# Kernel tuning notes

Measured on AMD Instinct MI355X. Metric: run time of the kernel, lower is better.

Reference implementation:

```python
import jax, jax.numpy as jnp
import numpy as np

B, S, H = 8, 1024, 1024
NH, HD = 16, 64
LN_EPS = 1e-12


def setup_inputs() -> dict:
    key = jax.random.key(0)
    ks = jax.random.split(key, 8)
    sd = 0.02
    return {
        "hidden_states": jax.random.normal(ks[0], (B, S, H), jnp.float32),
        "attention_mask": jnp.zeros((B, 1, 1, S), jnp.float32),
        "Wq": jax.random.normal(ks[1], (H, H), jnp.float32) * sd,
        "bq": jnp.zeros((H,), jnp.float32),
        "Wk": jax.random.normal(ks[2], (H, H), jnp.float32) * sd,
        "bk": jnp.zeros((H,), jnp.float32),
        "Wv": jax.random.normal(ks[3], (H, H), jnp.float32) * sd,
        "bv": jnp.zeros((H,), jnp.float32),
        "Wo": jax.random.normal(ks[4], (H, H), jnp.float32) * sd,
        "bo": jnp.zeros((H,), jnp.float32),
        "ln_gamma": jnp.ones((H,), jnp.float32),
        "ln_beta": jnp.zeros((H,), jnp.float32),
    }


def _heads(x):
    # [B,S,H] -> [B,NH,S,HD]
    return x.reshape(B, S, NH, HD).transpose(0, 2, 1, 3)


def reference(hidden_states, attention_mask, Wq, bq, Wk, bk, Wv, bv, Wo, bo, ln_gamma, ln_beta):
    # QKV projections (torch Linear: x @ W.T + b)
    q = _heads(hidden_states @ Wq.T + bq)
    k = _heads(hidden_states @ Wk.T + bk)
    v = _heads(hidden_states @ Wv.T + bv)
    # scaled dot-product attention with additive mask
    scores = jnp.einsum("bhqd,bhkd->bhqk", q, k) / np.sqrt(HD).astype(np.float32)
    scores = scores + attention_mask  # broadcast [B,1,1,S]
    probs = jax.nn.softmax(scores, axis=-1)
    ctx = jnp.einsum("bhqk,bhkd->bhqd", probs, v)
    ctx = ctx.transpose(0, 2, 1, 3).reshape(B, S, H)
    # output projection + residual + LayerNorm
    out = ctx @ Wo.T + bo
    x = out + hidden_states
    mu = jnp.mean(x, axis=-1, keepdims=True)
    var = jnp.var(x, axis=-1, keepdims=True)
    return (x - mu) * jax.lax.rsqrt(var + LN_EPS) * ln_gamma + ln_beta
```

## Files before the change

kernel.cpp:

```cpp
#include <hip/hip_runtime.h>
#include <stdint.h>

typedef __attribute__((ext_vector_type(8))) __bf16 bf16x8;
typedef __attribute__((ext_vector_type(8))) unsigned short ushortx8;
typedef __attribute__((ext_vector_type(4))) unsigned short ushortx4;
typedef __attribute__((ext_vector_type(4))) short short4v;
typedef __attribute__((ext_vector_type(4))) float floatx4;

#define LOG2E 1.4426950408889634f
#define QSCALE 0.18033688011112043f

#define ASYNC16(g, l) __builtin_amdgcn_global_load_lds( \
    (__attribute__((address_space(1))) void*)(g),       \
    (__attribute__((address_space(3))) void*)(l), 16, 0, 0)

__device__ __forceinline__ unsigned short f2bf(float f) {
    unsigned int u = __float_as_uint(f);
    u += 0x7fffu + ((u >> 16) & 1u);
    return (unsigned short)(u >> 16);
}
__device__ __forceinline__ float bf2f(unsigned short u) {
    return __uint_as_float((unsigned)u << 16);
}

__device__ __forceinline__ floatx4 mfma32(bf16x8 a, bf16x8 b, floatx4 c) {
    return __builtin_amdgcn_mfma_f32_16x16x32_bf16(a, b, c, 0, 0, 0);
}
__device__ __forceinline__ floatx4 mfma16(short4v a, short4v b, floatx4 c) {
    return __builtin_amdgcn_mfma_f32_16x16x16bf16_1k(a, b, c, 0, 0, 0);
}

__global__ __launch_bounds__(256) void cvt_all(
    const float* __restrict__ hidden,
    const float* __restrict__ Wq, const float* __restrict__ Wk,
    const float* __restrict__ Wv, const float* __restrict__ Wo,
    unsigned short* __restrict__ hid_bf,
    unsigned short* __restrict__ oqkv, unsigned short* __restrict__ oo)
{
    const float* src;
    unsigned short* dst;
    int i;
    if (blockIdx.x < 4096) {
        src = hidden; dst = hid_bf;
        i = blockIdx.x * 256 + threadIdx.x;
    } else {
        int blk = (blockIdx.x - 4096) >> 9;
        src = (blk == 0) ? Wq : (blk == 1) ? Wk : (blk == 2) ? Wv : Wo;
        dst = (blk == 3) ? oo : oqkv + (size_t)blk * 1048576;
        i = ((blockIdx.x - 4096) & 511) * 256 + threadIdx.x;
    }
    const float4* p = (const float4*)src + (size_t)i * 2;
    float4 a = p[0], b = p[1];
    ushortx8 o;
    o[0] = f2bf(a.x); o[1] = f2bf(a.y); o[2] = f2bf(a.z); o[3] = f2bf(a.w);
    o[4] = f2bf(b.x); o[5] = f2bf(b.y); o[6] = f2bf(b.z); o[7] = f2bf(b.w);
    *((ushortx8*)dst + i) = o;
}

template<bool SWAP>
__device__ __forceinline__ void kloop_bk64(
    const unsigned short* __restrict__ Ag,
    const unsigned short* __restrict__ Wg,
    unsigned short* As, unsigned short* Bs,
    int wm, int wn, int l16, int quad, int t,
    floatx4 acc[4][4])
{
#pragma unroll 1
    for (int k0 = 0; k0 < 1024; k0 += 64) {
        __syncthreads();
#pragma unroll
        for (int i = 0; i < 4; i++) {
            ASYNC16(Ag + (size_t)i * 32 * 1024 + k0, As + i * 2048 + t * 8);
            ASYNC16(Wg + (size_t)i * 32 * 1024 + k0, Bs + i * 2048 + t * 8);
        }
        __syncthreads();
#pragma unroll
        for (int s = 0; s < 2; s++) {
            int pb = ((s * 4 + quad) ^ (l16 & 7)) * 8;
            bf16x8 af[4], bfr[4];
#pragma unroll
            for (int mt = 0; mt < 4; mt++)
                af[mt] = *(const bf16x8*)(As + (wm + mt * 16 + l16) * 64 + pb);
#pragma unroll
            for (int nt = 0; nt < 4; nt++)
                bfr[nt] = *(const bf16x8*)(Bs + (wn + nt * 16 + l16) * 64 + pb);
            if (SWAP) {
#pragma unroll
                for (int ft = 0; ft < 4; ft++)
#pragma unroll
                    for (int st = 0; st < 4; st++)
                        acc[ft][st] = mfma32(bfr[ft], af[st], acc[ft][st]);
            } else {
#pragma unroll
                for (int mt = 0; mt < 4; mt++)
#pragma unroll
                    for (int nt = 0; nt < 4; nt++)
                        acc[mt][nt] = mfma32(af[mt], bfr[nt], acc[mt][nt]);
            }
        }
    }
}

__global__ __launch_bounds__(512, 2) void gemm_qkv(
    const unsigned short* __restrict__ A,
    const unsigned short* __restrict__ W,
    const float* __restrict__ bq, const float* __restrict__ bk, const float* __restrict__ bv,
    unsigned short* __restrict__ Qo, unsigned short* __restrict__ Ko,
    unsigned short* __restrict__ Vo)
{
    __shared__ unsigned short As[2][16384];
    __shared__ unsigned short Bs[2][12288];
    const int t = threadIdx.x;
    const int lane = t & 63, quad = lane >> 4, l16 = lane & 15;
    const int wid = t >> 6;
    const int wm = (wid >> 2) * 128;
    const int wn = (wid & 3) * 48;
    const int rr = t >> 3;
    const int cc = ((t & 7) ^ (rr & 7)) * 8;
    const int t8 = t * 8;

    const unsigned short* Ab = A + ((size_t)blockIdx.x * 256 + rr) * 1024 + cc;
    const unsigned short* Wb = W + ((size_t)blockIdx.y * 192 + rr) * 1024 + cc;

#define SA(bf_, u_, kt_) ASYNC16(Ab + (size_t)(u_) * 65536 + (kt_) * 64, &As[bf_][(u_) * 4096 + t8])
#define SB(bf_, u_, kt_) ASYNC16(Wb + (size_t)(u_) * 65536 + (kt_) * 64, &Bs[bf_][(u_) * 4096 + t8])

    SA(0, 0, 0); SA(0, 1, 0); SA(0, 2, 0); SA(0, 3, 0);
    SB(0, 0, 0); SB(0, 1, 0); SB(0, 2, 0);
    SB(1, 0, 1); SB(1, 1, 1); SB(1, 2, 1); SA(1, 0, 1); SA(1, 2, 1);
    asm volatile("s_waitcnt vmcnt(5)" ::: "memory");
    __builtin_amdgcn_s_barrier();

    floatx4 acc[3][8] = {};

#pragma unroll 1
    for (int kt = 0; kt < 16; ++kt) {
        const int cur = kt & 1, nb = cur ^ 1;
        const unsigned short* Ac = As[cur];
        const unsigned short* Bc = Bs[cur];
        bf16x8 bfr[3][2];
        bf16x8 af[4][2];

#pragma unroll
        for (int j = 0; j < 4; ++j)
#pragma unroll
            for (int s = 0; s < 2; ++s)
                af[j][s] = *(const bf16x8*)(Ac + (wm + j * 16 + l16) * 64 +
                                            ((s * 4 + quad) ^ (l16 & 7)) * 8);
#pragma unroll
        for (int ft = 0; ft < 3; ++ft)
#pragma unroll
            for (int s = 0; s < 2; ++s)
                bfr[ft][s] = *(const bf16x8*)(Bc + (wn + ft * 16 + l16) * 64 +
                                              ((s * 4 + quad) ^ (l16 & 7)) * 8);
        if (kt < 15) { SA(nb, 1, kt + 1); SA(nb, 3, kt + 1); }
        __builtin_amdgcn_s_barrier();
        asm volatile("s_waitcnt lgkmcnt(0)" ::: "memory");
        __builtin_amdgcn_sched_barrier(0);
        __builtin_amdgcn_s_setprio(1);
#pragma unroll
        for (int ft = 0; ft < 3; ++ft)
#pragma unroll
            for (int j = 0; j < 4; ++j) {
                acc[ft][j] = mfma32(bfr[ft][0], af[j][0], acc[ft][j]);
                acc[ft][j] = mfma32(bfr[ft][1], af[j][1], acc[ft][j]);
            }
        __builtin_amdgcn_s_setprio(0);
        __builtin_amdgcn_s_barrier();

#pragma unroll
        for (int j = 0; j < 4; ++j)
#pragma unroll
            for (int s = 0; s < 2; ++s)
                af[j][s] = *(const bf16x8*)(Ac + (wm + 64 + j * 16 + l16) * 64 +
                                            ((s * 4 + quad) ^ (l16 & 7)) * 8);
        if (kt < 14) {
            SB(cur, 0, kt + 2); SB(cur, 1, kt + 2); SB(cur, 2, kt + 2);
            SA(cur, 0, kt + 2); SA(cur, 2, kt + 2);
        }
        __builtin_amdgcn_s_barrier();
        asm volatile("s_waitcnt lgkmcnt(0)" ::: "memory");
        __builtin_amdgcn_sched_barrier(0);
        __builtin_amdgcn_s_setprio(1);
#pragma unroll
        for (int ft = 0; ft < 3; ++ft)
#pragma unroll
            for (int j = 0; j < 4; ++j) {
                acc[ft][4 + j] = mfma32(bfr[ft][0], af[j][0], acc[ft][4 + j]);
                acc[ft][4 + j] = mfma32(bfr[ft][1], af[j][1], acc[ft][4 + j]);
            }
        __builtin_amdgcn_s_setprio(0);
        if (kt < 14)       { asm volatile("s_waitcnt vmcnt(5)" ::: "memory"); }
        else if (kt == 14) { asm volatile("s_waitcnt vmcnt(0)" ::: "memory"); }
        if (kt < 15) __builtin_amdgcn_s_barrier();
    }
#undef SA
#undef SB

#pragma unroll
    for (int ft = 0; ft < 3; ++ft) {
        const int featg = blockIdx.y * 192 + wn + ft * 16 + quad * 4;
        const int mat = featg >> 10;
        const int fin = featg & 1023;
        if (mat < 2) {
            const float* bp = (mat == 0) ? bq : bk;
            unsigned short* op = (mat == 0) ? Qo : Ko;
            const float sc = (mat == 0) ? QSCALE : 1.0f;
            const float4 b4 = *(const float4*)(bp + fin);
            const int h = fin >> 6, d = fin & 63;
#pragma unroll
            for (int st = 0; st < 8; ++st) {
                const int sg = blockIdx.x * 256 + wm + st * 16 + l16;
                const int b = sg >> 10, s = sg & 1023;
                ushortx4 o4;
                o4[0] = f2bf((acc[ft][st][0] + b4.x) * sc);
                o4[1] = f2bf((acc[ft][st][1] + b4.y) * sc);
                o4[2] = f2bf((acc[ft][st][2] + b4.z) * sc);
                o4[3] = f2bf((acc[ft][st][3] + b4.w) * sc);
                *(ushortx4*)(op + (((size_t)(b * 16 + h) * 1024 + s) * 64 + d)) = o4;
            }
        } else {
            const float4 b4 = *(const float4*)(bv + fin);
#pragma unroll
            for (int r = 0; r < 4; ++r) {
                const int fr = fin + r;
                const int h = fr >> 6, d = fr & 63;
                const float bias = (r == 0) ? b4.x : (r == 1) ? b4.y : (r == 2) ? b4.z : b4.w;
#pragma unroll
                for (int st = 0; st < 8; ++st) {
                    const int sg = blockIdx.x * 256 + wm + st * 16 + l16;
                    const int b = sg >> 10, s = sg & 1023;
                    const int sp = (s & ~63) + ((st >> 1) & 1) * 32 + (l16 >> 2) * 8 +
                                   (st & 1) * 4 + (l16 & 3);
                    Vo[((size_t)(b * 16 + h) * 64 + d) * 1024 + sp] = f2bf(acc[ft][st][r] + bias);
                }
            }
        }
    }
}

__global__ __launch_bounds__(256) void attn(
    const unsigned short* __restrict__ Q,
    const unsigned short* __restrict__ Kg,
    const unsigned short* __restrict__ Vt,
    const float* __restrict__ mask,
    unsigned short* __restrict__ ctx)
{
    __shared__ unsigned short Ks[64 * 64];
    __shared__ unsigned short Vs[64 * 64];
    __shared__ float Msall[1024];

    const int t = threadIdx.x;
    const int wave = t >> 6, lane = t & 63, quad = lane >> 4, l16 = lane & 15;
    const int s7 = l16 & 7;
    const int head = blockIdx.x;
    const int b = head >> 4, h = head & 15;
    const int q0 = blockIdx.y * 128;
    const unsigned short* Qh = Q + (size_t)head * 65536;
    const unsigned short* Kh = Kg + (size_t)head * 65536;
    const unsigned short* Vh = Vt + (size_t)head * 65536;

    const int srow = t >> 3;
    const int scol = ((t & 7) ^ (srow & 7)) * 8;

    {
        float4 m4 = *(const float4*)(mask + b * 1024 + t * 4);
        m4.x *= LOG2E; m4.y *= LOG2E; m4.z *= LOG2E; m4.w *= LOG2E;
        *(float4*)(Msall + t * 4) = m4;
    }

    bf16x8 qf[2][2];
#pragma unroll
    for (int qg = 0; qg < 2; qg++) {
        const unsigned short* qp = Qh + (size_t)(q0 + wave * 32 + qg * 16 + l16) * 64 + quad * 8;
        qf[qg][0] = *(const bf16x8*)(qp);
        qf[qg][1] = *(const bf16x8*)(qp + 32);
    }

    const short4v ones = {(short)0x3F80, (short)0x3F80, (short)0x3F80, (short)0x3F80};
    floatx4 sum_acc[2] = {};
    floatx4 o_acc[2][4] = {};

    for (int k0 = 0; k0 < 1024; k0 += 64) {
        __syncthreads();
#pragma unroll
        for (int i = 0; i < 2; i++) {
            ASYNC16(Kh + (size_t)(k0 + i * 32 + srow) * 64 + scol, Ks + i * 2048 + t * 8);
            ASYNC16(Vh + (size_t)(i * 32 + srow) * 1024 + k0 + scol, Vs + i * 2048 + t * 8);
        }
        __syncthreads();

        short4v pf0[4], pf1[4];
#pragma unroll
        for (int nt = 0; nt < 4; nt++) {
            int krow = nt * 16 + l16;
            bf16x8 kf0 = *(const bf16x8*)(Ks + krow * 64 + ((quad ^ s7) * 8));
            bf16x8 kf1 = *(const bf16x8*)(Ks + krow * 64 + (((4 + quad) ^ s7) * 8));
            floatx4 mk = *(const floatx4*)(Msall + k0 + nt * 16 + quad * 4);
            floatx4 z0 = mk;
            z0 = mfma32(kf0, qf[0][0], z0);
            z0 = mfma32(kf1, qf[0][1], z0);
            floatx4 z1 = mk;
            z1 = mfma32(kf0, qf[1][0], z1);
            z1 = mfma32(kf1, qf[1][1], z1);
#pragma unroll
            for (int r = 0; r < 4; r++) {
                pf0[nt][r] = (short)(__float_as_uint(exp2f(z0[r])) >> 16);
                pf1[nt][r] = (short)(__float_as_uint(exp2f(z1[r])) >> 16);
            }
            sum_acc[0] = mfma16(ones, pf0[nt], sum_acc[0]);
            sum_acc[1] = mfma16(ones, pf1[nt], sum_acc[1]);
        }

#pragma unroll
        for (int dt = 0; dt < 4; dt++) {
            int vrow = dt * 16 + l16;
            ushortx8 v01 = *(const ushortx8*)(Vs + vrow * 64 + ((quad ^ s7) * 8));
            ushortx8 v23 = *(const ushortx8*)(Vs + vrow * 64 + (((4 + quad) ^ s7) * 8));
            short4v vf0 = {(short)v01[0], (short)v01[1], (short)v01[2], (short)v01[3]};
            short4v vf1 = {(short)v01[4], (short)v01[5], (short)v01[6], (short)v01[7]};
            short4v vf2 = {(short)v23[0], (short)v23[1], (short)v23[2], (short)v23[3]};
            short4v vf3 = {(short)v23[4], (short)v23[5], (short)v23[6], (short)v23[7]};
            o_acc[0][dt] = mfma16(vf0, pf0[0], o_acc[0][dt]);
            o_acc[0][dt] = mfma16(vf1, pf0[1], o_acc[0][dt]);
            o_acc[0][dt] = mfma16(vf2, pf0[2], o_acc[0][dt]);
            o_acc[0][dt] = mfma16(vf3, pf0[3], o_acc[0][dt]);
            o_acc[1][dt] = mfma16(vf0, pf1[0], o_acc[1][dt]);
            o_acc[1][dt] = mfma16(vf1, pf1[1], o_acc[1][dt]);
            o_acc[1][dt] = mfma16(vf2, pf1[2], o_acc[1][dt]);
            o_acc[1][dt] = mfma16(vf3, pf1[3], o_acc[1][dt]);
        }
    }

#pragma unroll
    for (int qg = 0; qg < 2; qg++) {
        float inv_l = 1.0f / sum_acc[qg][0];
        int qrow = q0 + wave * 32 + qg * 16 + l16;
#pragma unroll
        for (int dt = 0; dt < 4; dt++) {
            ushortx4 o4;
#pragma unroll
            for (int r = 0; r < 4; r++) o4[r] = f2bf(o_acc[qg][dt][r] * inv_l);
            *(ushortx4*)(ctx + ((size_t)(b * 1024 + qrow)) * 1024 + h * 64 + dt * 16 + quad * 4) = o4;
        }
    }
}

__global__ __launch_bounds__(256) void gemm_proj(
    const unsigned short* __restrict__ A,
    const unsigned short* __restrict__ W,
    const float* __restrict__ bo,
    const unsigned short* __restrict__ resid,
    unsigned short* __restrict__ X)
{
    __shared__ unsigned short As[128 * 64];
    __shared__ unsigned short Bs[128 * 64];
    const int t = threadIdx.x;
    const int wave = t >> 6, lane = t & 63;
    const int quad = lane >> 4, l16 = lane & 15;
    const int wm = (wave >> 1) * 64, wn = (wave & 1) * 64;
    const int srow = t >> 3;
    const int scol = ((t & 7) ^ (srow & 7)) * 8;

    const unsigned short* Ag = A + ((size_t)blockIdx.x * 128 + srow) * 1024 + scol;
    const unsigned short* Wg = W + ((size_t)blockIdx.y * 128 + srow) * 1024 + scol;

    floatx4 acc[4][4] = {};
    kloop_bk64<false>(Ag, Wg, As, Bs, wm, wn, l16, quad, t, acc);

#pragma unroll
    for (int nt = 0; nt < 4; nt++) {
        int gn = blockIdx.y * 128 + wn + nt * 16 + l16;
        float bias = bo[gn];
#pragma unroll
        for (int mt = 0; mt < 4; mt++) {
#pragma unroll
            for (int r = 0; r < 4; r++) {
                int gm = blockIdx.x * 128 + wm + mt * 16 + quad * 4 + r;
                size_t off = (size_t)gm * 1024 + gn;
                X[off] = f2bf(acc[mt][nt][r] + bias + bf2f(resid[off]));
            }
        }
    }
}

__global__ __launch_bounds__(256) void ln_k(const unsigned short* __restrict__ X,
                                            const float* __restrict__ g,
                                            const float* __restrict__ be,
                                            float* __restrict__ out)
{
    int row = blockIdx.x;
    int t = threadIdx.x;
    const unsigned short* xr = X + (size_t)row * 1024;
    ushortx4 xb = *(const ushortx4*)(xr + t * 4);
    float4 v;
    v.x = bf2f(xb[0]);
    v.y = bf2f(xb[1]);
    v.z = bf2f(xb[2]);
    v.w = bf2f(xb[3]);
    float s = v.x + v.y + v.z + v.w;
    float ss = v.x * v.x + v.y * v.y + v.z * v.z + v.w * v.w;
    for (int off = 1; off < 64; off <<= 1) {
        s += __shfl_xor(s, off);
        ss += __shfl_xor(ss, off);
    }
    __shared__ float red[8];
    int wave = t >> 6, lane = t & 63;
    if (lane == 0) { red[wave] = s; red[4 + wave] = ss; }
    __syncthreads();
    s = red[0] + red[1] + red[2] + red[3];
    ss = red[4] + red[5] + red[6] + red[7];
    float mu = s * (1.f / 1024.f);
    float var = ss * (1.f / 1024.f) - mu * mu;
    float inv = rsqrtf(var + 1e-12f);
    float4 gv = *(const float4*)(g + t * 4);
    float4 bv = *(const float4*)(be + t * 4);
    float4 o;
    o.x = (v.x - mu) * inv * gv.x + bv.x;
    o.y = (v.y - mu) * inv * gv.y + bv.y;
    o.z = (v.z - mu) * inv * gv.z + bv.z;
    o.w = (v.w - mu) * inv * gv.w + bv.w;
    *(float4*)(out + (size_t)row * 1024 + t * 4) = o;
}

extern "C" void kernel_launch(void* const* d_in, const int* in_sizes, int n_in,
                              void* d_out, int out_size, void* d_ws, size_t ws_size,
                              hipStream_t stream)
{
    const float* hidden = (const float*)d_in[0];
    const float* mask   = (const float*)d_in[1];
    const float* Wq = (const float*)d_in[2];
    const float* bq = (const float*)d_in[3];
    const float* Wk = (const float*)d_in[4];
    const float* bk = (const float*)d_in[5];
    const float* Wv = (const float*)d_in[6];
    const float* bv = (const float*)d_in[7];
    const float* Wo = (const float*)d_in[8];
    const float* bo = (const float*)d_in[9];
    const float* gamma = (const float*)d_in[10];
    const float* beta  = (const float*)d_in[11];
    float* out = (float*)d_out;

    char* ws = (char*)d_ws;
    unsigned short* hid_bf  = (unsigned short*)(ws + 0);
    unsigned short* wqkv_bf = (unsigned short*)(ws + 16777216);
    unsigned short* wo_bf   = (unsigned short*)(ws + 23068672);
    unsigned short* vt_bf   = (unsigned short*)(ws + 25165824);
    unsigned short* ctx_bf  = (unsigned short*)(ws + 41943040);
    unsigned short* q_bf    = (unsigned short*)(ws + 58720256);
    unsigned short* k_bf    = (unsigned short*)(ws + 75497472);
    unsigned short* x_bf    = (unsigned short*)(ws + 58720256);

    cvt_all<<<6144, 256, 0, stream>>>(hidden, Wq, Wk, Wv, Wo, hid_bf, wqkv_bf, wo_bf);

    gemm_qkv<<<dim3(32, 16), 512, 0, stream>>>(hid_bf, wqkv_bf, bq, bk, bv, q_bf, k_bf, vt_bf);
    attn<<<dim3(128, 8), 256, 0, stream>>>(q_bf, k_bf, vt_bf, mask, ctx_bf);
    gemm_proj<<<dim3(64, 8), 256, 0, stream>>>(ctx_bf, wo_bf, bo, hid_bf, x_bf);
    ln_k<<<8192, 256, 0, stream>>>(x_bf, gamma, beta, out);
}
```

Before: 260.4 us.

## Widen QKV GEMM block tile to 384 columns with two-phase B staging

Each QKV GEMM block now computes a 256x384 tile as two 192-column halves, holding two accumulator sets, so the grid halves to 32x8. The B tile is staged in two LDS buffers, one per half, and the loading of the other half overlaps with compute on the current one. The hand-tuned vmcnt waits, setprio and sched barriers are replaced by plain __syncthreads. The aim is to load each A tile once per 384 output columns instead of per 192, and to cut the block count to one wave. The cost is twice the accumulator registers, A fragments read from LDS twice, and possibly less latency hiding.

```diff
diff --git a/kernel.cpp b/kernel.cpp
--- a/kernel.cpp
+++ b/kernel.cpp
@@ -120,86 +120,66 @@
     const int t8 = t * 8;
 
     const unsigned short* Ab = A + ((size_t)blockIdx.x * 256 + rr) * 1024 + cc;
-    const unsigned short* Wb = W + ((size_t)blockIdx.y * 192 + rr) * 1024 + cc;
+    const unsigned short* Wb = W + ((size_t)blockIdx.y * 384 + rr) * 1024 + cc;
 
 #define SA(bf_, u_, kt_) ASYNC16(Ab + (size_t)(u_) * 65536 + (kt_) * 64, &As[bf_][(u_) * 4096 + t8])
-#define SB(bf_, u_, kt_) ASYNC16(Wb + (size_t)(u_) * 65536 + (kt_) * 64, &Bs[bf_][(u_) * 4096 + t8])
+#define SB(bf_, u_, rp_, kt_) ASYNC16(Wb + (size_t)(rp_) * 196608 + (size_t)(u_) * 65536 + (kt_) * 64, \
+                                      &Bs[bf_][(u_) * 4096 + t8])
 
     SA(0, 0, 0); SA(0, 1, 0); SA(0, 2, 0); SA(0, 3, 0);
-    SB(0, 0, 0); SB(0, 1, 0); SB(0, 2, 0);
-    SB(1, 0, 1); SB(1, 1, 1); SB(1, 2, 1); SA(1, 0, 1); SA(1, 2, 1);
-    asm volatile("s_waitcnt vmcnt(5)" ::: "memory");
-    __builtin_amdgcn_s_barrier();
-
-    floatx4 acc[3][8] = {};
+    SB(0, 0, 0, 0); SB(0, 1, 0, 0); SB(0, 2, 0, 0);
+    __syncthreads();
+
+    floatx4 acc[2][3][8] = {};
+
+#define REP_COMPUTE(RB)                                                              \
+    do {                                                                             \
+        bf16x8 bfr[3][2];                                                            \
+        _Pragma("unroll")                                                            \
+        for (int ft = 0; ft < 3; ++ft)                                               \
+            _Pragma("unroll")                                                        \
+            for (int s = 0; s < 2; ++s)                                              \
+                bfr[ft][s] = *(const bf16x8*)(Bs[RB] + (wn + ft * 16 + l16) * 64 +   \
+                                              ((s * 4 + quad) ^ (l16 & 7)) * 8);     \
+        _Pragma("unroll")                                                            \
+        for (int st = 0; st < 8; ++st) {                                             \
+            bf16x8 af0 = *(const bf16x8*)(Ac + (wm + st * 16 + l16) * 64 +           \
+                                          ((quad ^ (l16 & 7)) * 8));                 \
+            bf16x8 af1 = *(const bf16x8*)(Ac + (wm + st * 16 + l16) * 64 +           \
+                                          (((4 + quad) ^ (l16 & 7)) * 8));           \
+            _Pragma("unroll")                                                        \
+            for (int ft = 0; ft < 3; ++ft) {                                         \
+                acc[RB][ft][st] = mfma32(bfr[ft][0], af0, acc[RB][ft][st]);          \
+                acc[RB][ft][st] = mfma32(bfr[ft][1], af1, acc[RB][ft][st]);          \
+            }                                                                        \
+        }                                                                            \
+    } while (0)
 
 #pragma unroll 1
     for (int kt = 0; kt < 16; ++kt) {
-        const int cur = kt & 1, nb = cur ^ 1;
-        const unsigned short* Ac = As[cur];
-        const unsigned short* Bc = Bs[cur];
-        bf16x8 bfr[3][2];
-        bf16x8 af[4][2];
-
-#pragma unroll
-        for (int j = 0; j < 4; ++j)
-#pragma unroll
-            for (int s = 0; s < 2; ++s)
-                af[j][s] = *(const bf16x8*)(Ac + (wm + j * 16 + l16) * 64 +
-                                            ((s * 4 + quad) ^ (l16 & 7)) * 8);
-#pragma unroll
-        for (int ft = 0; ft < 3; ++ft)
-#pragma unroll
-            for (int s = 0; s < 2; ++s)
-                bfr[ft][s] = *(const bf16x8*)(Bc + (wn + ft * 16 + l16) * 64 +
-                                              ((s * 4 + quad) ^ (l16 & 7)) * 8);
-        if (kt < 15) { SA(nb, 1, kt + 1); SA(nb, 3, kt + 1); }
-        __builtin_amdgcn_s_barrier();
-        asm volatile("s_waitcnt lgkmcnt(0)" ::: "memory");
-        __builtin_amdgcn_sched_barrier(0);
-        __builtin_amdgcn_s_setprio(1);
-#pragma unroll
-        for (int ft = 0; ft < 3; ++ft)
-#pragma unroll
-            for (int j = 0; j < 4; ++j) {
-                acc[ft][j] = mfma32(bfr[ft][0], af[j][0], acc[ft][j]);
-                acc[ft][j] = mfma32(bfr[ft][1], af[j][1], acc[ft][j]);
-            }
-        __builtin_amdgcn_s_setprio(0);
-        __builtin_amdgcn_s_barrier();
-
-#pragma unroll
-        for (int j = 0; j < 4; ++j)
-#pragma unroll
-            for (int s = 0; s < 2; ++s)
-                af[j][s] = *(const bf16x8*)(Ac + (wm + 64 + j * 16 + l16) * 64 +
-                                            ((s * 4 + quad) ^ (l16 & 7)) * 8);
-        if (kt < 14) {
-            SB(cur, 0, kt + 2); SB(cur, 1, kt + 2); SB(cur, 2, kt + 2);
-            SA(cur, 0, kt + 2); SA(cur, 2, kt + 2);
-        }
-        __builtin_amdgcn_s_barrier();
-        asm volatile("s_waitcnt lgkmcnt(0)" ::: "memory");
-        __builtin_amdgcn_sched_barrier(0);
-        __builtin_amdgcn_s_setprio(1);
-#pragma unroll
-        for (int ft = 0; ft < 3; ++ft)
-#pragma unroll
-            for (int j = 0; j < 4; ++j) {
-                acc[ft][4 + j] = mfma32(bfr[ft][0], af[j][0], acc[ft][4 + j]);
-                acc[ft][4 + j] = mfma32(bfr[ft][1], af[j][1], acc[ft][4 + j]);
-            }
-        __builtin_amdgcn_s_setprio(0);
-        if (kt < 14)       { asm volatile("s_waitcnt vmcnt(5)" ::: "memory"); }
-        else if (kt == 14) { asm volatile("s_waitcnt vmcnt(0)" ::: "memory"); }
-        if (kt < 15) __builtin_amdgcn_s_barrier();
-    }
+        const int ab = kt & 1, nb = ab ^ 1;
+        const unsigned short* Ac = As[ab];
+
+        SB(1, 0, 1, kt); SB(1, 1, 1, kt); SB(1, 2, 1, kt);
+        REP_COMPUTE(0);
+        __syncthreads();
+
+        if (kt < 15) {
+            SA(nb, 0, kt + 1); SA(nb, 1, kt + 1); SA(nb, 2, kt + 1); SA(nb, 3, kt + 1);
+            SB(0, 0, 0, kt + 1); SB(0, 1, 0, kt + 1); SB(0, 2, 0, kt + 1);
+        }
+        REP_COMPUTE(1);
+        __syncthreads();
+    }
+#undef REP_COMPUTE
 #undef SA
 #undef SB
 
 #pragma unroll
+    for (int rp = 0; rp < 2; ++rp) {
+#pragma unroll
     for (int ft = 0; ft < 3; ++ft) {
-        const int featg = blockIdx.y * 192 + wn + ft * 16 + quad * 4;
+        const int featg = blockIdx.y * 384 + rp * 192 + wn + ft * 16 + quad * 4;
         const int mat = featg >> 10;
         const int fin = featg & 1023;
         if (mat < 2) {
@@ -213,10 +193,10 @@
                 const int sg = blockIdx.x * 256 + wm + st * 16 + l16;
                 const int b = sg >> 10, s = sg & 1023;
                 ushortx4 o4;
-                o4[0] = f2bf((acc[ft][st][0] + b4.x) * sc);
-                o4[1] = f2bf((acc[ft][st][1] + b4.y) * sc);
-                o4[2] = f2bf((acc[ft][st][2] + b4.z) * sc);
-                o4[3] = f2bf((acc[ft][st][3] + b4.w) * sc);
+                o4[0] = f2bf((acc[rp][ft][st][0] + b4.x) * sc);
+                o4[1] = f2bf((acc[rp][ft][st][1] + b4.y) * sc);
+                o4[2] = f2bf((acc[rp][ft][st][2] + b4.z) * sc);
+                o4[3] = f2bf((acc[rp][ft][st][3] + b4.w) * sc);
                 *(ushortx4*)(op + (((size_t)(b * 16 + h) * 1024 + s) * 64 + d)) = o4;
             }
         } else {
@@ -232,10 +212,11 @@
                     const int b = sg >> 10, s = sg & 1023;
                     const int sp = (s & ~63) + ((st >> 1) & 1) * 32 + (l16 >> 2) * 8 +
                                    (st & 1) * 4 + (l16 & 3);
-                    Vo[((size_t)(b * 16 + h) * 64 + d) * 1024 + sp] = f2bf(acc[ft][st][r] + bias);
+                    Vo[((size_t)(b * 16 + h) * 64 + d) * 1024 + sp] = f2bf(acc[rp][ft][st][r] + bias);
                 }
             }
         }
+    }
     }
 }
 
@@ -453,7 +434,7 @@
 
     cvt_all<<<6144, 256, 0, stream>>>(hidden, Wq, Wk, Wv, Wo, hid_bf, wqkv_bf, wo_bf);
 
-    gemm_qkv<<<dim3(32, 16), 512, 0, stream>>>(hid_bf, wqkv_bf, bq, bk, bv, q_bf, k_bf, vt_bf);
+    gemm_qkv<<<dim3(32, 8), 512, 0, stream>>>(hid_bf, wqkv_bf, bq, bk, bv, q_bf, k_bf, vt_bf);
     attn<<<dim3(128, 8), 256, 0, stream>>>(q_bf, k_bf, vt_bf, mask, ctx_bf);
     gemm_proj<<<dim3(64, 8), 256, 0, stream>>>(ctx_bf, wo_bf, bo, hid_bf, x_bf);
     ln_k<<<8192, 256, 0, stream>>>(x_bf, gamma, beta, out);
```

After: 263.6 us. Within noise of the previous version (+1.2%).
